# Kernel optimization log

Hardware: AMD Instinct MI355X
Metric: run time of the kernel (lower is better)

## Reference

```python
import jax, jax.numpy as jnp
import numpy as np
from jax import lax

B, TIN, N, TOUT, C = 8, 168, 1500, 24, 16
EMB, ALPHA, BETA, TOPK, DEPTH = 16, 1.5, 0.2, 12, 2
KERNELS = (2, 3, 6, 7)


def setup_inputs() -> dict:
    key = jax.random.key(0)
    ks = jax.random.split(key, 32)
    def rn(k, shape, scale=0.1):
        return jax.random.normal(k, shape, jnp.float32) * scale
    inp = {"x": jax.random.normal(ks[0], (B, TIN, N, 1), jnp.float32)}
    inp["pw"], inp["pb"] = rn(ks[1], (C, 1)), rn(ks[2], (C,))
    branch = C // len(KERNELS)
    for i, k in enumerate(KERNELS):
        inp[f"tw{k}"] = rn(ks[3 + 2 * i], (branch, C, 1, k))
        inp[f"tb{k}"] = rn(ks[4 + 2 * i], (branch,))
    inp["e1"], inp["e2"] = rn(ks[11], (N, EMB), 1.0), rn(ks[12], (N, EMB), 1.0)
    inp["gw1"], inp["gb1"] = rn(ks[13], (EMB, EMB)), rn(ks[14], (EMB,))
    inp["gw2"], inp["gb2"] = rn(ks[15], (EMB, EMB)), rn(ks[16], (EMB,))
    inp["mw"], inp["mb"] = rn(ks[17], (C, (DEPTH + 1) * C)), rn(ks[18], (C,))
    inp["rw1"], inp["rb1"] = rn(ks[19], (C, C)), rn(ks[20], (C,))
    inp["rw2"], inp["rb2"] = rn(ks[21], (TOUT, C)), rn(ks[22], (TOUT,))
    return inp


def _conv1x1(h, w, b):
    # h: [B, Cin, N, T], w: [Cout, Cin], b: [Cout]
    return jnp.einsum('bint,oi->bont', h, w) + b[None, :, None, None]


def _forward(x, pw, pb, tw2, tb2, tw3, tb3, tw6, tb6, tw7, tb7,
             e1, e2, gw1, gb1, gw2, gb2, mw, mb, rw1, rb1, rw2, rb2):
    h = jnp.transpose(x, (0, 3, 2, 1))                      # [B,1,N,TIN]
    h = _conv1x1(h, pw, pb)                                 # [B,C,N,TIN]
    # dilated inception: branches with kernels (2,3,6,7), truncate to shortest
    tlen = TIN - max(KERNELS) + 1
    outs = []
    for w, b in ((tw2, tb2), (tw3, tb3), (tw6, tb6), (tw7, tb7)):
        o = lax.conv_general_dilated(h, w, (1, 1), 'VALID',
                                     dimension_numbers=('NCHW', 'OIHW', 'NCHW'))
        outs.append(o[..., -tlen:] + b[None, :, None, None])
    h = jax.nn.relu(jnp.concatenate(outs, axis=1))          # [B,C,N,tlen]
    # adaptive top-k graph learning
    m1 = jnp.tanh(ALPHA * (e1 @ gw1 + gb1))
    m2 = jnp.tanh(ALPHA * (e2 @ gw2 + gb2))
    a = jax.nn.relu(jnp.tanh(ALPHA * (m1 @ m2.T - m2 @ m1.T)))  # [N,N]
    _, idx = lax.top_k(a, TOPK)
    mask = jnp.zeros((N, N), jnp.float32).at[jnp.arange(N)[:, None], idx].set(1.0)
    adj = a * mask
    # mix-hop graph convolution with row-normalized (A + I)
    adj = adj + jnp.eye(N, dtype=jnp.float32)
    adj = adj / jnp.sum(adj, axis=1, keepdims=True)
    hin = h
    hops = [h]
    for _ in range(DEPTH):
        h = BETA * hin + (1.0 - BETA) * jnp.einsum('bcwt,vw->bcvt', h, adj)
        hops.append(h)
    ho = jnp.concatenate(hops, axis=1)                      # [B,(D+1)C,N,tlen]
    h = jax.nn.relu(_conv1x1(ho, mw, mb))                   # [B,C,N,tlen]
    # dropout -> identity at inference
    r = jax.nn.relu(_conv1x1(h, rw1, rb1))
    y = _conv1x1(r, rw2, rb2)                               # [B,TOUT,N,tlen]
    return jnp.mean(y, axis=-1)                             # [B,TOUT,N]


def reference(x, pw, pb, tw2, tb2, tw3, tb3, tw6, tb6, tw7, tb7,
              e1, e2, gw1, gb1, gw2, gb2, mw, mb, rw1, rb1, rw2, rb2):
    return _forward(x, pw, pb, tw2, tb2, tw3, tb3, tw6, tb6, tw7, tb7,
                    e1, e2, gw1, gb1, gw2, gb2, mw, mb, rw1, rb1, rw2, rb2)
```

## Files before the change

kernel.cpp:

```cpp
#include <hip/hip_runtime.h>

#define BB 8
#define TIN 168
#define NN 1500
#define TOUTC 24
#define TLEN 162
#define NG 32
#define NTH 1024
#define SN 2
#define TOPKK 12
#define NTILE 94
#define NPAD 1504

#define OFF_M1   0
#define OFF_M2   24000
#define OFF_M1T  48000
#define OFF_M2T  72000
#define OFF_EW   96000
#define OFF_EB   96112
#define OFF_ADJ  96128
#define OFF_FR   135128
#define OFF_PART 328664

typedef __attribute__((ext_vector_type(8))) _Float16 half8;
typedef __attribute__((ext_vector_type(2))) _Float16 half2v;
typedef __attribute__((ext_vector_type(4))) float v4f;

__device__ __forceinline__ unsigned int pk2(float lo, float hi) {
    return __builtin_bit_cast(unsigned int, __builtin_amdgcn_cvt_pkrtz(lo, hi));
}
__device__ __forceinline__ float h2lo(unsigned int u) {
    return (float)__builtin_bit_cast(half2v, u).x;
}
__device__ __forceinline__ float h2hi(unsigned int u) {
    return (float)__builtin_bit_cast(half2v, u).y;
}
__device__ __forceinline__ half2v as_h2(unsigned int u) { return __builtin_bit_cast(half2v, u); }
__device__ __forceinline__ unsigned int as_u(half2v h) { return __builtin_bit_cast(unsigned int, h); }
__device__ __forceinline__ half8 as_h8(uint4 u) { return __builtin_bit_cast(half8, u); }

__global__ __launch_bounds__(256) void prep_kernel(
    const float* __restrict__ e1, const float* __restrict__ e2,
    const float* __restrict__ gw1, const float* __restrict__ gb1,
    const float* __restrict__ gw2, const float* __restrict__ gb2,
    const float* __restrict__ pw, const float* __restrict__ pb,
    const float* __restrict__ tw2, const float* __restrict__ tb2,
    const float* __restrict__ tw3, const float* __restrict__ tb3,
    const float* __restrict__ tw6, const float* __restrict__ tb6,
    const float* __restrict__ tw7, const float* __restrict__ tb7,
    const float* __restrict__ mw, const float* __restrict__ rw1,
    float* __restrict__ ws)
{
    int n = blockIdx.x * blockDim.x + threadIdx.x;
    if (n < NN) {
        float a1[16], a2[16];
        #pragma unroll
        for (int o = 0; o < 16; ++o) { a1[o] = gb1[o]; a2[o] = gb2[o]; }
        #pragma unroll
        for (int i = 0; i < 16; ++i) {
            float u = e1[n*16+i], v = e2[n*16+i];
            #pragma unroll
            for (int o = 0; o < 16; ++o) {
                a1[o] += u * gw1[i*16+o];
                a2[o] += v * gw2[i*16+o];
            }
        }
        #pragma unroll
        for (int o = 0; o < 16; ++o) {
            float t1v = tanhf(1.5f*a1[o]);
            float t2v = tanhf(1.5f*a2[o]);
            ws[OFF_M1 + n*16+o] = t1v;
            ws[OFF_M2 + n*16+o] = t2v;
            ws[OFF_M1T + o*NN + n] = t1v;
            ws[OFF_M2T + o*NN + n] = t2v;
        }
    }
    if (blockIdx.x == 0 && threadIdx.x < 16) {
        int c = threadIdx.x;
        int br = c >> 2, oc = c & 3;
        const float* tw; const float* tb; int k;
        if (br == 0)      { tw = tw2; tb = tb2; k = 2; }
        else if (br == 1) { tw = tw3; tb = tb3; k = 3; }
        else if (br == 2) { tw = tw6; tb = tb6; k = 6; }
        else              { tw = tw7; tb = tb7; k = 7; }
        for (int d = 0; d < 7; ++d) ws[OFF_EW + c*7 + d] = 0.f;
        float ebv = tb[oc];
        for (int j = 0; j < k; ++j) {
            float s = 0.f, sb = 0.f;
            for (int ic = 0; ic < 16; ++ic) {
                float w = tw[(oc*16+ic)*k + j];
                s  += w * pw[ic];
                sb += w * pb[ic];
            }
            ws[OFF_EW + c*7 + (7-k+j)] = s;
            ebv += sb;
        }
        ws[OFF_EB + c] = ebv;
    }
    if (blockIdx.x == 1 && threadIdx.x < 64) {
        int lane = threadIdx.x;
        int m = lane & 15, qq = lane >> 4;
        unsigned short* frw = (unsigned short*)(ws + OFF_FR);
        for (int mat = 0; mat < 3; ++mat) {
            for (int j = 0; j < 8; ++j) {
                int k = qq*8 + j;
                float s;
                if (mat == 0) s = (k < 16) ? mw[m*48+k] + 0.2f*(mw[m*48+16+k] + mw[m*48+32+k])
                                           : 0.8f*mw[m*48+16+(k-16)] + 0.16f*mw[m*48+32+(k-16)];
                else if (mat == 1) s = (k < 16) ? 0.64f*mw[m*48+32+k] : 0.f;
                else               s = (k < 16) ? rw1[m*16+k] : 0.f;
                _Float16 hi = (_Float16)s;
                _Float16 lo = (_Float16)(s - (float)hi);
                frw[(mat*2+0)*512 + lane*8 + j] = __builtin_bit_cast(unsigned short, hi);
                frw[(mat*2+1)*512 + lane*8 + j] = __builtin_bit_cast(unsigned short, lo);
            }
        }
    }
}

__global__ __launch_bounds__(256) void graph_kernel(
    const float* __restrict__ m1, const float* __restrict__ m2,
    const float* __restrict__ m1T, const float* __restrict__ m2T,
    int2* __restrict__ adj)
{
    int v = blockIdx.x;
    int tid = threadIdx.x;
    __shared__ float wv4[4];
    __shared__ int   wi4[4];
    __shared__ int   bcast_i;
    __shared__ float m1v[16], m2v[16];
    if (tid < 16) { m1v[tid] = m1[v*16+tid]; m2v[tid] = m2[v*16+tid]; }
    __syncthreads();
    float sreg[6];
    #pragma unroll
    for (int u = 0; u < 6; ++u) {
        int j = tid + 256*u;
        float a = -1.f;
        if (j < NN) {
            float d = 0.f;
            #pragma unroll
            for (int i = 0; i < 16; ++i)
                d += m1v[i]*m2T[i*NN+j] - m2v[i]*m1T[i*NN+j];
            float t = tanhf(1.5f*d);
            a = t > 0.f ? t : 0.f;
        }
        sreg[u] = a;
    }
    float lb = -1.f; int li = NN;
    #pragma unroll
    for (int u = 0; u < 6; ++u) {
        int j = tid + 256*u;
        if (j < NN && sreg[u] > lb) { lb = sreg[u]; li = j; }
    }
    const int wid = tid >> 6;
    float kw[TOPKK]; int ki[TOPKK];
    #pragma unroll
    for (int it = 0; it < TOPKK; ++it) {
        float bv = lb; int bi = li;
        #pragma unroll
        for (int off = 32; off > 0; off >>= 1) {
            float ov = __shfl_down(bv, off);
            int   oi = __shfl_down(bi, off);
            if (ov > bv || (ov == bv && oi < bi)) { bv = ov; bi = oi; }
        }
        if ((tid & 63) == 0) { wv4[wid] = bv; wi4[wid] = bi; }
        __syncthreads();
        if (tid == 0) {
            #pragma unroll
            for (int w = 1; w < 4; ++w) {
                float ov = wv4[w]; int oi = wi4[w];
                if (ov > bv || (ov == bv && oi < bi)) { bv = ov; bi = oi; }
            }
            kw[it] = bv; ki[it] = bi;
            bcast_i = bi;
        }
        __syncthreads();
        int win = bcast_i;
        if (li == win) {
            #pragma unroll
            for (int u = 0; u < 6; ++u)
                if (tid + 256*u == win) sreg[u] = -1.f;
            lb = -1.f; li = NN;
            #pragma unroll
            for (int u = 0; u < 6; ++u) {
                int j = tid + 256*u;
                if (j < NN && sreg[u] > lb) { lb = sreg[u]; li = j; }
            }
        }
    }
    if (tid == 0) {
        float s = 1.f;
        #pragma unroll
        for (int it = 0; it < TOPKK; ++it) s += kw[it];
        float inv = 1.f/s;
        float w13[13]; int i13[13];
        #pragma unroll
        for (int it = 0; it < TOPKK; ++it) { w13[it] = kw[it]*inv; i13[it] = ki[it]; }
        w13[12] = inv; i13[12] = v;
        for (int a = 1; a < 13; ++a) {
            float wv = w13[a]; int iv = i13[a]; int key = iv & 7;
            int c = a - 1;
            while (c >= 0 && (i13[c] & 7) > key) { w13[c+1] = w13[c]; i13[c+1] = i13[c]; --c; }
            w13[c+1] = wv; i13[c+1] = iv;
        }
        int rot = v % 13;
        for (int j = 0; j < 13; ++j) {
            int sidx = j + rot; if (sidx >= 13) sidx -= 13;
            adj[j*NN + v] = make_int2((int)pk2(w13[sidx], w13[sidx]), i13[sidx]);
        }
    }
}

__device__ __forceinline__ half8 ldfrag(const unsigned short* fr, int plane, int lane) {
    const uint4* p = (const uint4*)(fr + plane*512);
    return as_h8(p[lane]);
}

__global__ __launch_bounds__(NTH, 4) void main_kernel(
    const float* __restrict__ x,
    const float* __restrict__ ew, const float* __restrict__ eb,
    const int2* __restrict__ adj,
    const unsigned short* __restrict__ fr,
    unsigned int* __restrict__ part,
    const float* __restrict__ mb, const float* __restrict__ rb1)
{
    __shared__ uint4 feat[6][NPAD];

    const int tid = threadIdx.x;
    const int lane = tid & 63;
    const int wid = tid >> 6;
    const int b = blockIdx.x >> 5;
    const int g = blockIdx.x & 31;
    const int t0 = (g*TLEN) >> 5;
    const int t1 = ((g+1)*TLEN) >> 5;
    const int n0 = lane & 15, q = lane >> 4;
    unsigned int* partBG = part + (size_t)(b*NG + g)*NN*8;

    #pragma unroll 1
    for (int s = 0; s < SN; ++s) {
        int v = tid + NTH*s;
        if (v < NN) {
            float xv[7];
            #pragma unroll
            for (int d = 0; d < 7; ++d) xv[d] = x[(b*TIN + t0 + d)*NN + v];
            float h[16];
            #pragma unroll
            for (int c = 0; c < 16; ++c) {
                float a = eb[c];
                #pragma unroll
                for (int d = 0; d < 7; ++d) a += ew[c*7+d]*xv[d];
                h[c] = a > 0.f ? a : 0.f;
            }
            feat[0][v] = make_uint4(pk2(h[0],h[1]), pk2(h[2],h[3]), pk2(h[4],h[5]), pk2(h[6],h[7]));
            feat[1][v] = make_uint4(pk2(h[8],h[9]), pk2(h[10],h[11]), pk2(h[12],h[13]), pk2(h[14],h[15]));
        }
    }
    __syncthreads();

    for (int t = t0; t < t1; ++t) {
        const int par = (t - t0) & 1;
        const int hc = par ? 4 : 0;
        const int hn = par ? 0 : 4;

        #pragma unroll 1
        for (int s = 0; s < SN; ++s) {
            int v = tid + NTH*s;
            if (v < NN) {
                const half2v zero = {(_Float16)0.f, (_Float16)0.f};
                half2v acc[8];
                #pragma unroll
                for (int i = 0; i < 8; ++i) acc[i] = zero;
                #pragma unroll
                for (int j = 0; j < 13; ++j) {
                    int2 aw = adj[j*NN + v];
                    half2v w2 = as_h2((unsigned int)aw.x);
                    int nb = aw.y;
                    uint4 b0 = feat[hc][nb], b1 = feat[hc+1][nb];
                    acc[0] = as_h2(b0.x) * w2 + acc[0];
                    acc[1] = as_h2(b0.y) * w2 + acc[1];
                    acc[2] = as_h2(b0.z) * w2 + acc[2];
                    acc[3] = as_h2(b0.w) * w2 + acc[3];
                    acc[4] = as_h2(b1.x) * w2 + acc[4];
                    acc[5] = as_h2(b1.y) * w2 + acc[5];
                    acc[6] = as_h2(b1.z) * w2 + acc[6];
                    acc[7] = as_h2(b1.w) * w2 + acc[7];
                }
                feat[2][v] = make_uint4(as_u(acc[0]), as_u(acc[1]), as_u(acc[2]), as_u(acc[3]));
                feat[3][v] = make_uint4(as_u(acc[4]), as_u(acc[5]), as_u(acc[6]), as_u(acc[7]));
            }
        }
        __syncthreads();

        {
            half8 a1h = ldfrag(fr, 0, lane), a1l = ldfrag(fr, 1, lane);
            half8 a2h = ldfrag(fr, 2, lane), a2l = ldfrag(fr, 3, lane);
            uint2* zH = (uint2*)feat[hc + (q >> 1)];
            uint2* pH = (uint2*)feat[2  + (q >> 1)];
            #pragma unroll 1
            for (int T = wid; T < NTILE; T += 16) {
                int n = T*16 + n0;
                half8 bf  = as_h8(feat[(q < 2) ? (hc + q) : q][n]);
                half8 b2f = as_h8(feat[2 + (q & 1)][n]);
                v4f z = {0.f,0.f,0.f,0.f}, p = {0.f,0.f,0.f,0.f};
                z = __builtin_amdgcn_mfma_f32_16x16x32_f16(a1h, bf, z, 0, 0, 0);
                z = __builtin_amdgcn_mfma_f32_16x16x32_f16(a1l, bf, z, 0, 0, 0);
                p = __builtin_amdgcn_mfma_f32_16x16x32_f16(a2h, b2f, p, 0, 0, 0);
                p = __builtin_amdgcn_mfma_f32_16x16x32_f16(a2l, b2f, p, 0, 0, 0);
                uint2 zz; zz.x = pk2(z[0], z[1]); zz.y = pk2(z[2], z[3]);
                uint2 pp; pp.x = pk2(p[0], p[1]); pp.y = pk2(p[2], p[3]);
                zH[n*2 + (q & 1)] = zz;
                pH[n*2 + (q & 1)] = pp;
            }
        }
        __syncthreads();

        if (t + 1 < t1) {
            #pragma unroll 1
            for (int s = 0; s < SN; ++s) {
                int v = tid + NTH*s;
                if (v < NN) {
                    float xv[7];
                    #pragma unroll
                    for (int d = 0; d < 7; ++d) xv[d] = x[(b*TIN + (t+1) + d)*NN + v];
                    float h[16];
                    #pragma unroll
                    for (int c = 0; c < 16; ++c) {
                        float a = eb[c];
                        #pragma unroll
                        for (int d = 0; d < 7; ++d) a += ew[c*7+d]*xv[d];
                        h[c] = a > 0.f ? a : 0.f;
                    }
                    feat[hn][v]   = make_uint4(pk2(h[0],h[1]), pk2(h[2],h[3]), pk2(h[4],h[5]), pk2(h[6],h[7]));
                    feat[hn+1][v] = make_uint4(pk2(h[8],h[9]), pk2(h[10],h[11]), pk2(h[12],h[13]), pk2(h[14],h[15]));
                }
            }
        }
        {
            half8 a3h = ldfrag(fr, 4, lane), a3l = ldfrag(fr, 5, lane);
            float mbq[4], rbq[4];
            #pragma unroll
            for (int r = 0; r < 4; ++r) { mbq[r] = mb[q*4+r]; rbq[r] = rb1[q*4+r]; }
            uint2* zH = (uint2*)feat[hc + (q >> 1)];
            const uint2* pH = (const uint2*)feat[2 + (q >> 1)];
            #pragma unroll 1
            for (int T = wid; T < NTILE; T += 16) {
                int n = T*16 + n0;
                uint2 zz = zH[n*2 + (q & 1)];
                int vc = n < NN ? n : NN-1;
                const half2v zero = {(_Float16)0.f, (_Float16)0.f};
                half2v ga = zero, gb = zero;
                #pragma unroll
                for (int j = 0; j < 13; ++j) {
                    int2 aw = adj[j*NN + vc];
                    half2v w2 = as_h2((unsigned int)aw.x);
                    int nb = aw.y;
                    uint2 ps = pH[nb*2 + (q & 1)];
                    ga = as_h2(ps.x) * w2 + ga;
                    gb = as_h2(ps.y) * w2 + gb;
                }
                float y0 = mbq[0] + h2lo(zz.x) + (float)ga.x;
                float y1 = mbq[1] + h2hi(zz.x) + (float)ga.y;
                float y2 = mbq[2] + h2lo(zz.y) + (float)gb.x;
                float y3 = mbq[3] + h2hi(zz.y) + (float)gb.y;
                y0 = y0 > 0.f ? y0 : 0.f;  y1 = y1 > 0.f ? y1 : 0.f;
                y2 = y2 > 0.f ? y2 : 0.f;  y3 = y3 > 0.f ? y3 : 0.f;
                uint2 ypk; ypk.x = pk2(y0, y1); ypk.y = pk2(y2, y3);
                zH[n*2 + (q & 1)] = ypk;
                asm volatile("" ::: "memory");
                half8 bfY = as_h8(feat[(q < 2) ? (hc + q) : q][n]);
                v4f acc = {0.f,0.f,0.f,0.f};
                acc = __builtin_amdgcn_mfma_f32_16x16x32_f16(a3h, bfY, acc, 0, 0, 0);
                acc = __builtin_amdgcn_mfma_f32_16x16x32_f16(a3l, bfY, acc, 0, 0, 0);
                if (n < NN) {
                    float r0 = acc[0]+rbq[0], r1 = acc[1]+rbq[1], r2 = acc[2]+rbq[2], r3 = acc[3]+rbq[3];
                    r0 = r0 > 0.f ? r0 : 0.f;  r1 = r1 > 0.f ? r1 : 0.f;
                    r2 = r2 > 0.f ? r2 : 0.f;  r3 = r3 > 0.f ? r3 : 0.f;
                    uint2 nv; nv.x = pk2(r0, r1); nv.y = pk2(r2, r3);
                    uint2* pp = (uint2*)(partBG + (size_t)n*8 + q*2);
                    if (t == t0) {
                        *pp = nv;
                    } else {
                        uint2 o = *pp;
                        uint2 m;
                        m.x = as_u(as_h2(o.x) + as_h2(nv.x));
                        m.y = as_u(as_h2(o.y) + as_h2(nv.y));
                        *pp = m;
                    }
                }
            }
        }
        __syncthreads();
    }
}

__global__ __launch_bounds__(256) void reduce_kernel(const unsigned int* __restrict__ part,
                                                     const float* __restrict__ rw2,
                                                     const float* __restrict__ rb2,
                                                     float* __restrict__ out)
{
    int idx = blockIdx.x*256 + threadIdx.x;
    if (idx >= BB*NN) return;
    int v = idx % NN;
    int b = idx / NN;
    float s[16];
    #pragma unroll
    for (int c = 0; c < 16; ++c) s[c] = 0.f;
    #pragma unroll 4
    for (int g = 0; g < NG; ++g) {
        const uint4* p4 = (const uint4*)(part + ((size_t)(b*NG + g)*NN + v)*8);
        uint4 u0 = p4[0], u1 = p4[1];
        s[0] += h2lo(u0.x); s[1] += h2hi(u0.x); s[2]  += h2lo(u0.y); s[3]  += h2hi(u0.y);
        s[4] += h2lo(u0.z); s[5] += h2hi(u0.z); s[6]  += h2lo(u0.w); s[7]  += h2hi(u0.w);
        s[8] += h2lo(u1.x); s[9] += h2hi(u1.x); s[10] += h2lo(u1.y); s[11] += h2hi(u1.y);
        s[12]+= h2lo(u1.z); s[13]+= h2hi(u1.z); s[14] += h2lo(u1.w); s[15] += h2hi(u1.w);
    }
    #pragma unroll
    for (int c = 0; c < 16; ++c) s[c] *= (1.0f/TLEN);
    #pragma unroll
    for (int o = 0; o < TOUTC; ++o) {
        float a = rb2[o];
        #pragma unroll
        for (int c = 0; c < 16; ++c) a += rw2[o*16+c]*s[c];
        out[(b*TOUTC + o)*NN + v] = a;
    }
}

extern "C" void kernel_launch(void* const* d_in, const int* in_sizes, int n_in,
                              void* d_out, int out_size, void* d_ws, size_t ws_size,
                              hipStream_t stream)
{
    const float* x   = (const float*)d_in[0];
    const float* pw  = (const float*)d_in[1];
    const float* pb  = (const float*)d_in[2];
    const float* tw2 = (const float*)d_in[3];
    const float* tb2 = (const float*)d_in[4];
    const float* tw3 = (const float*)d_in[5];
    const float* tb3 = (const float*)d_in[6];
    const float* tw6 = (const float*)d_in[7];
    const float* tb6 = (const float*)d_in[8];
    const float* tw7 = (const float*)d_in[9];
    const float* tb7 = (const float*)d_in[10];
    const float* e1  = (const float*)d_in[11];
    const float* e2  = (const float*)d_in[12];
    const float* gw1 = (const float*)d_in[13];
    const float* gb1 = (const float*)d_in[14];
    const float* gw2 = (const float*)d_in[15];
    const float* gb2 = (const float*)d_in[16];
    const float* mw  = (const float*)d_in[17];
    const float* mb  = (const float*)d_in[18];
    const float* rw1 = (const float*)d_in[19];
    const float* rb1 = (const float*)d_in[20];
    const float* rw2 = (const float*)d_in[21];
    const float* rb2 = (const float*)d_in[22];
    float* ws  = (float*)d_ws;
    float* out = (float*)d_out;

    prep_kernel<<<(NN + 255)/256, 256, 0, stream>>>(e1,e2,gw1,gb1,gw2,gb2,pw,pb,
                                                    tw2,tb2,tw3,tb3,tw6,tb6,tw7,tb7,
                                                    mw, rw1, ws);
    graph_kernel<<<NN, 256, 0, stream>>>(ws + OFF_M1, ws + OFF_M2,
                                         ws + OFF_M1T, ws + OFF_M2T,
                                         (int2*)(ws + OFF_ADJ));
    main_kernel<<<BB*NG, NTH, 0, stream>>>(x, ws + OFF_EW, ws + OFF_EB,
                                           (const int2*)(ws + OFF_ADJ),
                                           (const unsigned short*)(ws + OFF_FR),
                                           (unsigned int*)(ws + OFF_PART), mb, rb1);
    reduce_kernel<<<(BB*NN + 255)/256, 256, 0, stream>>>((const unsigned int*)(ws + OFF_PART),
                                                         rw2, rb2, out);
}
```

Measured before the change: 298.1 us.

## Fuse mix-conv MFMA pass into final graph hop and drop adjacency sorting

Removes the separate per-timestep MFMA pass (and its barrier) that precomputed z and p into shared memory. z is now computed inline in the final loop, and the gathered second hop is multiplied by the hop-2 mixing weights with a 16x16x16 MFMA on registers. The y result is also fed straight into the residual MFMA from registers instead of through an LDS round trip. Separately, the graph kernel no longer sorts and rotates neighbours by index&7, so writes are simpler but the LDS gather loses its bank-conflict-avoiding order.

```diff
diff --git a/kernel.cpp b/kernel.cpp
--- a/kernel.cpp
+++ b/kernel.cpp
@@ -23,6 +23,7 @@
 #define OFF_PART 328664
 
 typedef __attribute__((ext_vector_type(8))) _Float16 half8;
+typedef __attribute__((ext_vector_type(4))) _Float16 half4v;
 typedef __attribute__((ext_vector_type(2))) _Float16 half2v;
 typedef __attribute__((ext_vector_type(4))) float v4f;
 
@@ -101,19 +102,27 @@
         int lane = threadIdx.x;
         int m = lane & 15, qq = lane >> 4;
         unsigned short* frw = (unsigned short*)(ws + OFF_FR);
-        for (int mat = 0; mat < 3; ++mat) {
-            for (int j = 0; j < 8; ++j) {
-                int k = qq*8 + j;
-                float s;
-                if (mat == 0) s = (k < 16) ? mw[m*48+k] + 0.2f*(mw[m*48+16+k] + mw[m*48+32+k])
-                                           : 0.8f*mw[m*48+16+(k-16)] + 0.16f*mw[m*48+32+(k-16)];
-                else if (mat == 1) s = (k < 16) ? 0.64f*mw[m*48+32+k] : 0.f;
-                else               s = (k < 16) ? rw1[m*16+k] : 0.f;
-                _Float16 hi = (_Float16)s;
-                _Float16 lo = (_Float16)(s - (float)hi);
-                frw[(mat*2+0)*512 + lane*8 + j] = __builtin_bit_cast(unsigned short, hi);
-                frw[(mat*2+1)*512 + lane*8 + j] = __builtin_bit_cast(unsigned short, lo);
-            }
+        for (int j = 0; j < 8; ++j) {
+            int k = qq*8 + j;
+            float s = (k < 16) ? mw[m*48+k] + 0.2f*(mw[m*48+16+k] + mw[m*48+32+k])
+                               : 0.8f*mw[m*48+16+(k-16)] + 0.16f*mw[m*48+32+(k-16)];
+            _Float16 hi = (_Float16)s;
+            _Float16 lo = (_Float16)(s - (float)hi);
+            frw[0*512 + lane*8 + j] = __builtin_bit_cast(unsigned short, hi);
+            frw[1*512 + lane*8 + j] = __builtin_bit_cast(unsigned short, lo);
+        }
+        for (int j = 0; j < 4; ++j) {
+            int k = qq*4 + j;
+            float sv = 0.64f*mw[m*48+32+k];
+            float sr = rw1[m*16+k];
+            _Float16 vhi = (_Float16)sv;
+            _Float16 vlo = (_Float16)(sv - (float)vhi);
+            _Float16 rhi = (_Float16)sr;
+            _Float16 rlo = (_Float16)(sr - (float)rhi);
+            frw[2*512 + lane*4 + j] = __builtin_bit_cast(unsigned short, vhi);
+            frw[3*512 + lane*4 + j] = __builtin_bit_cast(unsigned short, vlo);
+            frw[4*512 + lane*4 + j] = __builtin_bit_cast(unsigned short, rhi);
+            frw[5*512 + lane*4 + j] = __builtin_bit_cast(unsigned short, rlo);
         }
     }
 }
@@ -193,27 +202,22 @@
         #pragma unroll
         for (int it = 0; it < TOPKK; ++it) s += kw[it];
         float inv = 1.f/s;
-        float w13[13]; int i13[13];
-        #pragma unroll
-        for (int it = 0; it < TOPKK; ++it) { w13[it] = kw[it]*inv; i13[it] = ki[it]; }
-        w13[12] = inv; i13[12] = v;
-        for (int a = 1; a < 13; ++a) {
-            float wv = w13[a]; int iv = i13[a]; int key = iv & 7;
-            int c = a - 1;
-            while (c >= 0 && (i13[c] & 7) > key) { w13[c+1] = w13[c]; i13[c+1] = i13[c]; --c; }
-            w13[c+1] = wv; i13[c+1] = iv;
-        }
-        int rot = v % 13;
-        for (int j = 0; j < 13; ++j) {
-            int sidx = j + rot; if (sidx >= 13) sidx -= 13;
-            adj[j*NN + v] = make_int2((int)pk2(w13[sidx], w13[sidx]), i13[sidx]);
-        }
+        #pragma unroll
+        for (int it = 0; it < TOPKK; ++it) {
+            float w = kw[it]*inv;
+            adj[it*NN + v] = make_int2((int)pk2(w, w), ki[it]);
+        }
+        adj[TOPKK*NN + v] = make_int2((int)pk2(inv, inv), v);
     }
 }
 
 __device__ __forceinline__ half8 ldfrag(const unsigned short* fr, int plane, int lane) {
     const uint4* p = (const uint4*)(fr + plane*512);
     return as_h8(p[lane]);
+}
+__device__ __forceinline__ half4v ldfrag4(const unsigned short* fr, int plane, int lane) {
+    const uint2* p = (const uint2*)(fr + plane*512);
+    return __builtin_bit_cast(half4v, p[lane]);
 }
 
 __global__ __launch_bounds__(NTH, 4) void main_kernel(
@@ -291,29 +295,6 @@
         }
         __syncthreads();
 
-        {
-            half8 a1h = ldfrag(fr, 0, lane), a1l = ldfrag(fr, 1, lane);
-            half8 a2h = ldfrag(fr, 2, lane), a2l = ldfrag(fr, 3, lane);
-            uint2* zH = (uint2*)feat[hc + (q >> 1)];
-            uint2* pH = (uint2*)feat[2  + (q >> 1)];
-            #pragma unroll 1
-            for (int T = wid; T < NTILE; T += 16) {
-                int n = T*16 + n0;
-                half8 bf  = as_h8(feat[(q < 2) ? (hc + q) : q][n]);
-                half8 b2f = as_h8(feat[2 + (q & 1)][n]);
-                v4f z = {0.f,0.f,0.f,0.f}, p = {0.f,0.f,0.f,0.f};
-                z = __builtin_amdgcn_mfma_f32_16x16x32_f16(a1h, bf, z, 0, 0, 0);
-                z = __builtin_amdgcn_mfma_f32_16x16x32_f16(a1l, bf, z, 0, 0, 0);
-                p = __builtin_amdgcn_mfma_f32_16x16x32_f16(a2h, b2f, p, 0, 0, 0);
-                p = __builtin_amdgcn_mfma_f32_16x16x32_f16(a2l, b2f, p, 0, 0, 0);
-                uint2 zz; zz.x = pk2(z[0], z[1]); zz.y = pk2(z[2], z[3]);
-                uint2 pp; pp.x = pk2(p[0], p[1]); pp.y = pk2(p[2], p[3]);
-                zH[n*2 + (q & 1)] = zz;
-                pH[n*2 + (q & 1)] = pp;
-            }
-        }
-        __syncthreads();
-
         if (t + 1 < t1) {
             #pragma unroll 1
             for (int s = 0; s < SN; ++s) {
@@ -336,16 +317,20 @@
             }
         }
         {
-            half8 a3h = ldfrag(fr, 4, lane), a3l = ldfrag(fr, 5, lane);
+            half8  a1h = ldfrag(fr, 0, lane),  a1l = ldfrag(fr, 1, lane);
+            half4v v2h = ldfrag4(fr, 2, lane), v2l = ldfrag4(fr, 3, lane);
+            half4v r1h = ldfrag4(fr, 4, lane), r1l = ldfrag4(fr, 5, lane);
             float mbq[4], rbq[4];
             #pragma unroll
             for (int r = 0; r < 4; ++r) { mbq[r] = mb[q*4+r]; rbq[r] = rb1[q*4+r]; }
-            uint2* zH = (uint2*)feat[hc + (q >> 1)];
-            const uint2* pH = (const uint2*)feat[2 + (q >> 1)];
+            const uint2* uH = (const uint2*)feat[2 + (q >> 1)];
             #pragma unroll 1
             for (int T = wid; T < NTILE; T += 16) {
                 int n = T*16 + n0;
-                uint2 zz = zH[n*2 + (q & 1)];
+                half8 bf = as_h8(feat[(q < 2) ? (hc + q) : q][n]);
+                v4f z = {0.f,0.f,0.f,0.f};
+                z = __builtin_amdgcn_mfma_f32_16x16x32_f16(a1h, bf, z, 0, 0, 0);
+                z = __builtin_amdgcn_mfma_f32_16x16x32_f16(a1l, bf, z, 0, 0, 0);
                 int vc = n < NN ? n : NN-1;
                 const half2v zero = {(_Float16)0.f, (_Float16)0.f};
                 half2v ga = zero, gb = zero;
@@ -354,23 +339,25 @@
                     int2 aw = adj[j*NN + vc];
                     half2v w2 = as_h2((unsigned int)aw.x);
                     int nb = aw.y;
-                    uint2 ps = pH[nb*2 + (q & 1)];
+                    uint2 ps = uH[nb*2 + (q & 1)];
                     ga = as_h2(ps.x) * w2 + ga;
                     gb = as_h2(ps.y) * w2 + gb;
                 }
-                float y0 = mbq[0] + h2lo(zz.x) + (float)ga.x;
-                float y1 = mbq[1] + h2hi(zz.x) + (float)ga.y;
-                float y2 = mbq[2] + h2lo(zz.y) + (float)gb.x;
-                float y3 = mbq[3] + h2hi(zz.y) + (float)gb.y;
+                half4v w4 = {ga.x, ga.y, gb.x, gb.y};
+                v4f sv = {0.f,0.f,0.f,0.f};
+                sv = __builtin_amdgcn_mfma_f32_16x16x16f16(v2h, w4, sv, 0, 0, 0);
+                sv = __builtin_amdgcn_mfma_f32_16x16x16f16(v2l, w4, sv, 0, 0, 0);
+                float y0 = mbq[0] + z[0] + sv[0];
+                float y1 = mbq[1] + z[1] + sv[1];
+                float y2 = mbq[2] + z[2] + sv[2];
+                float y3 = mbq[3] + z[3] + sv[3];
                 y0 = y0 > 0.f ? y0 : 0.f;  y1 = y1 > 0.f ? y1 : 0.f;
                 y2 = y2 > 0.f ? y2 : 0.f;  y3 = y3 > 0.f ? y3 : 0.f;
-                uint2 ypk; ypk.x = pk2(y0, y1); ypk.y = pk2(y2, y3);
-                zH[n*2 + (q & 1)] = ypk;
-                asm volatile("" ::: "memory");
-                half8 bfY = as_h8(feat[(q < 2) ? (hc + q) : q][n]);
+                uint2 yk; yk.x = pk2(y0, y1); yk.y = pk2(y2, y3);
+                half4v y4 = __builtin_bit_cast(half4v, yk);
                 v4f acc = {0.f,0.f,0.f,0.f};
-                acc = __builtin_amdgcn_mfma_f32_16x16x32_f16(a3h, bfY, acc, 0, 0, 0);
-                acc = __builtin_amdgcn_mfma_f32_16x16x32_f16(a3l, bfY, acc, 0, 0, 0);
+                acc = __builtin_amdgcn_mfma_f32_16x16x16f16(r1h, y4, acc, 0, 0, 0);
+                acc = __builtin_amdgcn_mfma_f32_16x16x16f16(r1l, y4, acc, 0, 0, 0);
                 if (n < NN) {
                     float r0 = acc[0]+rbq[0], r1 = acc[1]+rbq[1], r2 = acc[2]+rbq[2], r3 = acc[3]+rbq[3];
                     r0 = r0 > 0.f ? r0 : 0.f;  r1 = r1 > 0.f ? r1 : 0.f;
```

After: 281.4 us. 5.6% less time.
